# Kernel optimization log

Measured on AMD Instinct MI355X. Metric: run time of the kernel, lower is better.

Reference implementation:

```python
import jax, jax.numpy as jnp
import numpy as np

B, T, D, W = 2, 8192, 2048, 128  # batch, seq, n_embd, local_window
PAD = -1.0


def setup_inputs() -> dict:
    key = jax.random.key(0)
    k1, k2, k3 = jax.random.split(key, 3)
    x = jax.random.normal(k1, (B, T, D), jnp.float32)
    w_attn = jax.random.normal(k2, (3 * D, D), jnp.float32) * 0.02  # nn.Linear(n_embd, 3*n_embd)
    w_o = jax.random.normal(k3, (D, D), jnp.float32) * 0.02        # o_proj
    return {"x": x, "w_attn": w_attn, "w_o": w_o}


def reference(x, w_attn, w_o):
    Bn, Tn, Dn = x.shape
    w = Tn // W  # number of windows

    qkv = x @ w_attn.T                      # [B,T,3D]
    q, k, v = jnp.split(qkv, 3, axis=-1)
    q = q / W                               # q / config.local_window

    bq = q.reshape(Bn, w, W, Dn)
    bk = k.reshape(Bn, w, W, Dn)
    bv = v.reshape(Bn, w, W, Dn)

    # look_around(backward=1, forward=0, pad_value=-1): keys = [prev_window, cur_window]
    pad_blk = jnp.full((Bn, 1, W, Dn), PAD, dtype=x.dtype)
    bk_prev = jnp.concatenate([pad_blk, bk[:, :-1]], axis=1)
    bv_prev = jnp.concatenate([pad_blk, bv[:, :-1]], axis=1)
    bk2 = jnp.concatenate([bk_prev, bk], axis=2)  # [B,w,2W,D]
    bv2 = jnp.concatenate([bv_prev, bv], axis=2)  # [B,w,2W,D]

    # position indices
    t = jnp.arange(Tn, dtype=jnp.int32).reshape(w, W)
    t_prev = jnp.concatenate([jnp.full((1, W), -1, jnp.int32), t[:-1]], axis=0)
    tj = jnp.concatenate([t_prev, t], axis=1)     # [w,2W] key positions (-1 = pad)
    ti = t[:, :, None]                            # [w,W,1] query positions
    tjb = tj[:, None, :]                          # [w,1,2W]

    # masked where (ti < tj) | (ti > tj + W) | pad; masked sim -> 0 (not -inf; relu2, no softmax)
    keep = (ti >= tjb) & (ti <= tjb + W) & (tjb != -1)  # [w,W,2W]

    sim = jnp.einsum('bwie,bwje->bwij', bq, bk2)        # [B,w,W,2W]
    sim = jnp.where(keep[None], sim, 0.0)
    attn = jnp.square(jax.nn.relu(sim))                 # relu^2, no normalization
    out = jnp.einsum('bwij,bwje->bwie', attn, bv2)      # [B,w,W,D]
    out = out.reshape(Bn, Tn, Dn)
    return out @ w_o.T
```

## Files before the change

kernel.cpp:

```cpp
#include <hip/hip_runtime.h>
#include <stdint.h>
#include <stddef.h>

#define Bn 2
#define Tn 8192
#define Dn 2048

typedef unsigned short u16;
typedef unsigned int u32;
typedef __attribute__((ext_vector_type(8))) short short8;
typedef __attribute__((ext_vector_type(8))) unsigned short u16x8;
typedef __attribute__((ext_vector_type(4))) float f32x4;

__device__ __forceinline__ u16 f2bf(float f) {
  u32 x = __builtin_bit_cast(u32, f);
  x += 0x7fffu + ((x >> 16) & 1u);
  return (u16)(x >> 16);
}

__device__ __forceinline__ void gload16(void* lds, const void* g) {
  __builtin_amdgcn_global_load_lds(
      (const __attribute__((address_space(1))) u32*)g,
      (__attribute__((address_space(3))) u32*)lds, 16, 0, 0);
}

#define PH_BAR asm volatile("s_barrier" ::: "memory")
#define WAITV(N) asm volatile("s_waitcnt vmcnt(" #N ")" ::: "memory")

__global__ void cast_kernel(const float* __restrict__ in, u16* __restrict__ out, int n) {
  int stride = gridDim.x * blockDim.x;
  for (int i = blockIdx.x * blockDim.x + threadIdx.x; i < (n >> 2); i += stride) {
    float4 v = reinterpret_cast<const float4*>(in)[i];
    ushort4 o;
    o.x = f2bf(v.x); o.y = f2bf(v.y); o.z = f2bf(v.z); o.w = f2bf(v.w);
    reinterpret_cast<ushort4*>(out)[i] = o;
  }
}

template <int MODE>
__global__ __launch_bounds__(512, 2) void gemm256(
    const u16* __restrict__ Ag, const u16* __restrict__ Bg,
    u16* __restrict__ Oq, u16* __restrict__ Ok, u16* __restrict__ Ov,
    float* __restrict__ Of, int K) {
  __shared__ char sh[131072];
  const int tid = threadIdx.x, lane = tid & 63, wid = tid >> 6;
  const int wm = wid >> 2, wn = wid & 3;
  const int fr = lane & 15, kk = (lane >> 4) * 8;
  const int NT = K >> 6;

  int lin = blockIdx.y * 64 + blockIdx.x;
  int nwg = gridDim.x * gridDim.y;
  int lin2 = (lin & 7) * (nwg >> 3) + (lin >> 3);
  const int m0 = (lin2 & 63) * 256;
  const int n0 = (lin2 >> 6) * 256;

  const int rdoff = (fr * 128 + kk * 2) ^ (((fr >> 2) & 1) << 5);
  const int lq = (lane * 16) ^ (((lane >> 5) & 1) << 5);
  const int stgrow = wid * 8 + (lq >> 7);
  const int stgcol = (lq & 127) >> 1;

  auto stageA = [&](int db, int h, int tt) {
    const u16* s = Ag + (size_t)(m0 + h * 128 + stgrow) * K + tt * 64 + stgcol;
    char* d = sh + db * 32768 + h * 16384 + wid * 1024;
    gload16(d, s);
    gload16(d + 8192, s + (size_t)64 * K);
  };
  auto stageB = [&](int db, int h, int tt) {
    const u16* s = Bg + (size_t)(n0 + h * 128 + stgrow) * K + tt * 64 + stgcol;
    char* d = sh + 65536 + db * 32768 + h * 16384 + wid * 1024;
    gload16(d, s);
    gload16(d + 8192, s + (size_t)64 * K);
  };

  short8 a[4][2], b0[2][2], b1[2][2];
  f32x4 acc[8][4] = {};

  stageA(0, 0, 0); stageA(0, 1, 0); stageB(0, 0, 0); stageB(0, 1, 0);
  stageB(1, 0, 1); stageB(1, 1, 1);
  WAITV(4);
  PH_BAR;

  for (int t = 0; t < NT; ++t) {
    const int db = t & 1;
    const char* rdA = sh + db * 32768 + wm * 16384 + rdoff;
    const char* rdB = sh + 65536 + db * 32768 + (wn >> 1) * 16384 + (wn & 1) * 8192 + rdoff;

#pragma unroll
    for (int fm = 0; fm < 4; ++fm)
#pragma unroll
      for (int ks = 0; ks < 2; ++ks)
        a[fm][ks] = *(const short8*)(rdA + fm * 2048 + ks * 64);
#pragma unroll
    for (int fn = 0; fn < 2; ++fn)
#pragma unroll
      for (int ks = 0; ks < 2; ++ks)
        b0[fn][ks] = *(const short8*)(rdB + fn * 2048 + ks * 64);
    if (t + 1 < NT) stageA(db ^ 1, 0, t + 1);
    PH_BAR;
    __builtin_amdgcn_s_setprio(1);
#pragma unroll
    for (int fm = 0; fm < 4; ++fm)
#pragma unroll
      for (int fn = 0; fn < 2; ++fn)
#pragma unroll
        for (int ks = 0; ks < 2; ++ks)
          acc[fm][fn] = __builtin_amdgcn_mfma_f32_16x16x32_bf16(a[fm][ks], b0[fn][ks], acc[fm][fn], 0, 0, 0);
    __builtin_amdgcn_s_setprio(0);
    PH_BAR;

#pragma unroll
    for (int fn = 0; fn < 2; ++fn)
#pragma unroll
      for (int ks = 0; ks < 2; ++ks)
        b1[fn][ks] = *(const short8*)(rdB + (2 + fn) * 2048 + ks * 64);
    if (t + 1 < NT) stageA(db ^ 1, 1, t + 1);
    PH_BAR;
    __builtin_amdgcn_s_setprio(1);
#pragma unroll
    for (int fm = 0; fm < 4; ++fm)
#pragma unroll
      for (int fn = 0; fn < 2; ++fn)
#pragma unroll
        for (int ks = 0; ks < 2; ++ks)
          acc[fm][2 + fn] = __builtin_amdgcn_mfma_f32_16x16x32_bf16(a[fm][ks], b1[fn][ks], acc[fm][2 + fn], 0, 0, 0);
    __builtin_amdgcn_s_setprio(0);
    PH_BAR;

#pragma unroll
    for (int fm = 0; fm < 4; ++fm)
#pragma unroll
      for (int ks = 0; ks < 2; ++ks)
        a[fm][ks] = *(const short8*)(rdA + (4 + fm) * 2048 + ks * 64);
    if (t + 2 < NT) stageB(db, 0, t + 2);
    PH_BAR;
    __builtin_amdgcn_s_setprio(1);
#pragma unroll
    for (int fm = 0; fm < 4; ++fm)
#pragma unroll
      for (int fn = 0; fn < 2; ++fn)
#pragma unroll
        for (int ks = 0; ks < 2; ++ks)
          acc[4 + fm][fn] = __builtin_amdgcn_mfma_f32_16x16x32_bf16(a[fm][ks], b0[fn][ks], acc[4 + fm][fn], 0, 0, 0);
    __builtin_amdgcn_s_setprio(0);
    PH_BAR;

    if (t + 2 < NT) stageB(db, 1, t + 2);
    PH_BAR;
    __builtin_amdgcn_s_setprio(1);
#pragma unroll
    for (int fm = 0; fm < 4; ++fm)
#pragma unroll
      for (int fn = 0; fn < 2; ++fn)
#pragma unroll
        for (int ks = 0; ks < 2; ++ks)
          acc[4 + fm][2 + fn] = __builtin_amdgcn_mfma_f32_16x16x32_bf16(a[fm][ks], b1[fn][ks], acc[4 + fm][2 + fn], 0, 0, 0);
    __builtin_amdgcn_s_setprio(0);
    if (t + 2 < NT) { WAITV(4); }
    else if (t + 1 < NT) { WAITV(0); }
    PH_BAR;
  }

  const int ci = (lane >> 4) * 4;
  if (MODE == 0) {
    const int seg = n0 >> 11;
    u16* Cb = (seg == 0) ? Oq : ((seg == 1) ? Ok : Ov);
    const float scale = (seg == 0) ? (1.0f / 128.0f) : 1.0f;
    const int nl0 = n0 & (Dn - 1);
#pragma unroll
    for (int fm = 0; fm < 8; ++fm)
#pragma unroll
      for (int fn = 0; fn < 4; ++fn) {
        int row = m0 + wm * 128 + fm * 16 + ci;
        int col = nl0 + wn * 64 + fn * 16 + fr;
#pragma unroll
        for (int r = 0; r < 4; ++r)
          Cb[(size_t)(row + r) * Dn + col] = f2bf(acc[fm][fn][r] * scale);
      }
  } else {
#pragma unroll
    for (int fm = 0; fm < 8; ++fm)
#pragma unroll
      for (int fn = 0; fn < 4; ++fn) {
        int row = m0 + wm * 128 + fm * 16 + ci;
        int col = n0 + wn * 64 + fn * 16 + fr;
#pragma unroll
        for (int r = 0; r < 4; ++r)
          Of[(size_t)(row + r) * Dn + col] = acc[fm][fn][r];
      }
  }
}

__global__ __launch_bounds__(256) void transpose_kernel(
    const u16* __restrict__ vin, u16* __restrict__ vout) {
  __shared__ u16 tile[64][72];
  const int b = blockIdx.z;
  const int t0 = blockIdx.x * 64, d0 = blockIdx.y * 64;
  const int tid = threadIdx.x;
#pragma unroll
  for (int i = 0; i < 2; ++i) {
    int chunk = tid + i * 256;
    int row = chunk >> 3;
    int col = (chunk & 7) * 8;
    u16x8 v = *reinterpret_cast<const u16x8*>(
        vin + ((size_t)b * Tn + t0 + row) * Dn + d0 + col);
#pragma unroll
    for (int j = 0; j < 8; ++j) tile[row][col + j] = v[j];
  }
  __syncthreads();
#pragma unroll
  for (int i = 0; i < 2; ++i) {
    int chunk = tid + i * 256;
    int drow = chunk >> 3;
    int tcol = (chunk & 7) * 8;
    u16x8 v;
#pragma unroll
    for (int j = 0; j < 8; ++j) v[j] = tile[tcol + j][drow];
    *reinterpret_cast<u16x8*>(vout + ((size_t)b * Dn + d0 + drow) * Tn + t0 + tcol) = v;
  }
}

__global__ __launch_bounds__(512) void attn_kernel(
    const u16* __restrict__ q, const u16* __restrict__ k,
    const u16* __restrict__ vT, u16* __restrict__ ao) {
  __shared__ u16 sStage[16384];
  __shared__ u16 sP[128 * 264];
  u16* Qs = sStage;
  u16* Ks = sStage + 4096;
  u16* Vts = sStage;

  const int bid = blockIdx.x;
  const int b = bid >> 6, blk = bid & 63;
  const int tid = threadIdx.x, lane = tid & 63, wid = tid >> 6;
  const int tprev = blk * 128 - 128;

  const u16* qp = q + ((size_t)b * Tn + blk * 128) * Dn;
  const u16* kp = k + (size_t)b * Tn * Dn;
  const u16* vp = vT + (size_t)b * Dn * Tn;

  const int wm = wid >> 2, wn = wid & 3;
  const int srow = lane >> 2, scol = (lane & 3) * 8;
  const int fr = lane & 15, kk = (lane >> 4) * 8;

  f32x4 acc[4][4] = {};
  for (int k0 = 0; k0 < Dn; k0 += 32) {
    {
      int row = wid * 16 + srow;
      gload16(Qs + wid * 512, qp + (size_t)row * Dn + k0 + scol);
    }
#pragma unroll
    for (int i = 0; i < 2; ++i) {
      int chunk = wid * 2 + i;
      int j = chunk * 16 + srow;
      int trow = tprev + j;
      if (trow < 0) trow = 0;
      gload16(Ks + chunk * 512, kp + (size_t)trow * Dn + k0 + scol);
    }
    __syncthreads();
    short8 av[4], bv[4];
#pragma unroll
    for (int f = 0; f < 4; ++f) {
      av[f] = *reinterpret_cast<const short8*>(&Qs[(wm * 64 + f * 16 + fr) * 32 + kk]);
      bv[f] = *reinterpret_cast<const short8*>(&Ks[(wn * 64 + f * 16 + fr) * 32 + kk]);
    }
#pragma unroll
    for (int fm = 0; fm < 4; ++fm)
#pragma unroll
      for (int fn = 0; fn < 4; ++fn)
        acc[fm][fn] = __builtin_amdgcn_mfma_f32_16x16x32_bf16(av[fm], bv[fn], acc[fm][fn], 0, 0, 0);
    __syncthreads();
  }

  {
    const int ci = (lane >> 4) * 4;
#pragma unroll
    for (int fm = 0; fm < 4; ++fm)
#pragma unroll
      for (int fn = 0; fn < 4; ++fn)
#pragma unroll
        for (int r = 0; r < 4; ++r) {
          int i = wm * 64 + fm * 16 + ci + r;
          int j = wn * 64 + fn * 16 + fr;
          float s = acc[fm][fn][r];
          bool keep = (j < 128) ? (blk > 0 && i <= j) : (i >= j - 128);
          float p = (keep && s > 0.0f) ? s * s : 0.0f;
          sP[i * 264 + j] = f2bf(p);
        }
  }
  __syncthreads();

  for (int c = 0; c < 32; ++c) {
#pragma unroll
    for (int i = 0; i < 4; ++i) {
      int chunk = wid * 4 + i;
      int d = c * 64 + chunk * 2 + (lane >> 5);
      int t = tprev + (lane & 31) * 8;
      if (t < 0) t = 0;
      gload16(Vts + chunk * 512, vp + (size_t)d * Tn + t);
    }
    __syncthreads();
    f32x4 pacc[4] = {};
#pragma unroll
    for (int ks = 0; ks < 8; ++ks) {
      short8 a = *reinterpret_cast<const short8*>(&sP[(wid * 16 + fr) * 264 + ks * 32 + kk]);
#pragma unroll
      for (int fn = 0; fn < 4; ++fn) {
        short8 bv2 = *reinterpret_cast<const short8*>(&Vts[(fn * 16 + fr) * 256 + ks * 32 + kk]);
        pacc[fn] = __builtin_amdgcn_mfma_f32_16x16x32_bf16(a, bv2, pacc[fn], 0, 0, 0);
      }
    }
    const int ci = (lane >> 4) * 4;
    int trow = blk * 128 + wid * 16 + ci;
#pragma unroll
    for (int fn = 0; fn < 4; ++fn) {
      int d = c * 64 + fn * 16 + fr;
#pragma unroll
      for (int r = 0; r < 4; ++r)
        ao[((size_t)b * Tn + trow + r) * Dn + d] = f2bf(pacc[fn][r]);
    }
    __syncthreads();
  }
}

extern "C" void kernel_launch(void* const* d_in, const int* in_sizes, int n_in,
                              void* d_out, int out_size, void* d_ws, size_t ws_size,
                              hipStream_t stream) {
  const float* x = (const float*)d_in[0];
  const float* w_attn = (const float*)d_in[1];
  const float* w_o = (const float*)d_in[2];
  float* out = (float*)d_out;

  char* ws = (char*)d_ws;
  u16* xb  = (u16*)(ws + 0);
  u16* wb  = (u16*)(ws + 67108864);
  u16* wob = (u16*)(ws + 92274688);
  u16* qb  = (u16*)(ws + 100663296);
  u16* kb  = (u16*)(ws + 167772160);
  u16* vb  = (u16*)(ws + 234881024);
  u16* vTb = xb;
  u16* ao  = vb;

  cast_kernel<<<2048, 256, 0, stream>>>(x, xb, Bn * Tn * Dn);
  cast_kernel<<<1024, 256, 0, stream>>>(w_attn, wb, 3 * Dn * Dn);
  cast_kernel<<<512, 256, 0, stream>>>(w_o, wob, Dn * Dn);

  gemm256<0><<<dim3(64, 24), 512, 0, stream>>>(xb, wb, qb, kb, vb, nullptr, Dn);

  transpose_kernel<<<dim3(128, 32, 2), 256, 0, stream>>>(vb, vTb);

  attn_kernel<<<128, 512, 0, stream>>>(qb, kb, vTb, ao);

  gemm256<1><<<dim3(64, 8), 512, 0, stream>>>(ao, wob, nullptr, nullptr, nullptr, out, Dn);
}
```

Baseline: 1.030 ms.

## XOR-swizzle LDS layouts in GEMM and attention; widen attention QK k-step to 64

Replaces the LDS staging layouts in the GEMM and the attention kernel with an XOR swizzle of 16-byte chunks across rows, and adjusts the MFMA fragment read offsets to match. The aim is to cut LDS bank conflicts on the short8 fragment reads. The attention QK loop now steps 64 columns of K per iteration instead of 32, with a larger staging buffer, which halves the barrier count in that loop. The PV stage reads V tiles through the same swizzle. The new index math is intricate and a wrong swizzle would silently corrupt results.

```diff
diff --git a/kernel.cpp b/kernel.cpp
--- a/kernel.cpp
+++ b/kernel.cpp
@@ -45,7 +45,7 @@
   __shared__ char sh[131072];
   const int tid = threadIdx.x, lane = tid & 63, wid = tid >> 6;
   const int wm = wid >> 2, wn = wid & 3;
-  const int fr = lane & 15, kk = (lane >> 4) * 8;
+  const int fr = lane & 15;
   const int NT = K >> 6;
 
   int lin = blockIdx.y * 64 + blockIdx.x;
@@ -54,19 +54,23 @@
   const int m0 = (lin2 & 63) * 256;
   const int n0 = (lin2 >> 6) * 256;
 
-  const int rdoff = (fr * 128 + kk * 2) ^ (((fr >> 2) & 1) << 5);
-  const int lq = (lane * 16) ^ (((lane >> 5) & 1) << 5);
-  const int stgrow = wid * 8 + (lq >> 7);
-  const int stgcol = (lq & 127) >> 1;
+  const int frb2 = (fr >> 2) & 1;
+  const int kkb = (lane >> 4) * 16;
+  const int rdoff = fr * 128 + (kkb ^ ((fr & 3) << 4));
+  const int koff0 = frb2 * 64;
+  const int koff1 = 64 - koff0;
+
+  const int srow8 = lane >> 3;
+  const int scol8 = ((lane & 7) ^ srow8) * 8;
 
   auto stageA = [&](int db, int h, int tt) {
-    const u16* s = Ag + (size_t)(m0 + h * 128 + stgrow) * K + tt * 64 + stgcol;
+    const u16* s = Ag + (size_t)(m0 + h * 128 + wid * 8 + srow8) * K + tt * 64 + scol8;
     char* d = sh + db * 32768 + h * 16384 + wid * 1024;
     gload16(d, s);
     gload16(d + 8192, s + (size_t)64 * K);
   };
   auto stageB = [&](int db, int h, int tt) {
-    const u16* s = Bg + (size_t)(n0 + h * 128 + stgrow) * K + tt * 64 + stgcol;
+    const u16* s = Bg + (size_t)(n0 + h * 128 + wid * 8 + srow8) * K + tt * 64 + scol8;
     char* d = sh + 65536 + db * 32768 + h * 16384 + wid * 1024;
     gload16(d, s);
     gload16(d + 8192, s + (size_t)64 * K);
@@ -89,12 +93,12 @@
     for (int fm = 0; fm < 4; ++fm)
 #pragma unroll
       for (int ks = 0; ks < 2; ++ks)
-        a[fm][ks] = *(const short8*)(rdA + fm * 2048 + ks * 64);
+        a[fm][ks] = *(const short8*)(rdA + fm * 2048 + (ks ? koff1 : koff0));
 #pragma unroll
     for (int fn = 0; fn < 2; ++fn)
 #pragma unroll
       for (int ks = 0; ks < 2; ++ks)
-        b0[fn][ks] = *(const short8*)(rdB + fn * 2048 + ks * 64);
+        b0[fn][ks] = *(const short8*)(rdB + fn * 2048 + (ks ? koff1 : koff0));
     if (t + 1 < NT) stageA(db ^ 1, 0, t + 1);
     PH_BAR;
     __builtin_amdgcn_s_setprio(1);
@@ -112,7 +116,7 @@
     for (int fn = 0; fn < 2; ++fn)
 #pragma unroll
       for (int ks = 0; ks < 2; ++ks)
-        b1[fn][ks] = *(const short8*)(rdB + (2 + fn) * 2048 + ks * 64);
+        b1[fn][ks] = *(const short8*)(rdB + (2 + fn) * 2048 + (ks ? koff1 : koff0));
     if (t + 1 < NT) stageA(db ^ 1, 1, t + 1);
     PH_BAR;
     __builtin_amdgcn_s_setprio(1);
@@ -130,7 +134,7 @@
     for (int fm = 0; fm < 4; ++fm)
 #pragma unroll
       for (int ks = 0; ks < 2; ++ks)
-        a[fm][ks] = *(const short8*)(rdA + (4 + fm) * 2048 + ks * 64);
+        a[fm][ks] = *(const short8*)(rdA + (4 + fm) * 2048 + (ks ? koff1 : koff0));
     if (t + 2 < NT) stageB(db, 0, t + 2);
     PH_BAR;
     __builtin_amdgcn_s_setprio(1);
@@ -222,10 +226,10 @@
 __global__ __launch_bounds__(512) void attn_kernel(
     const u16* __restrict__ q, const u16* __restrict__ k,
     const u16* __restrict__ vT, u16* __restrict__ ao) {
-  __shared__ u16 sStage[16384];
+  __shared__ u16 sStage[24576];
   __shared__ u16 sP[128 * 264];
   u16* Qs = sStage;
-  u16* Ks = sStage + 4096;
+  u16* Ks = sStage + 8192;
   u16* Vts = sStage;
 
   const int bid = blockIdx.x;
@@ -238,35 +242,49 @@
   const u16* vp = vT + (size_t)b * Dn * Tn;
 
   const int wm = wid >> 2, wn = wid & 3;
-  const int srow = lane >> 2, scol = (lane & 3) * 8;
-  const int fr = lane & 15, kk = (lane >> 4) * 8;
+  const int fr = lane & 15;
+  const int kkb = (lane >> 4) * 16;
+
+  const int frb2 = (fr >> 2) & 1;
+  const int rdoff = fr * 128 + (kkb ^ ((fr & 3) << 4));
+  const int koff0 = frb2 * 64;
+  const int koff1 = 64 - koff0;
+  const int srow8 = lane >> 3;
+  const int scol8 = ((lane & 7) ^ srow8) * 8;
 
   f32x4 acc[4][4] = {};
-  for (int k0 = 0; k0 < Dn; k0 += 32) {
-    {
-      int row = wid * 16 + srow;
-      gload16(Qs + wid * 512, qp + (size_t)row * Dn + k0 + scol);
-    }
+  for (int k0 = 0; k0 < Dn; k0 += 64) {
 #pragma unroll
     for (int i = 0; i < 2; ++i) {
       int chunk = wid * 2 + i;
-      int j = chunk * 16 + srow;
-      int trow = tprev + j;
+      int row = chunk * 8 + srow8;
+      gload16((char*)Qs + chunk * 1024, qp + (size_t)row * Dn + k0 + scol8);
+    }
+#pragma unroll
+    for (int i = 0; i < 4; ++i) {
+      int chunk = wid * 4 + i;
+      int trow = tprev + chunk * 8 + srow8;
       if (trow < 0) trow = 0;
-      gload16(Ks + chunk * 512, kp + (size_t)trow * Dn + k0 + scol);
+      gload16((char*)Ks + chunk * 1024, kp + (size_t)trow * Dn + k0 + scol8);
     }
     __syncthreads();
-    short8 av[4], bv[4];
-#pragma unroll
-    for (int f = 0; f < 4; ++f) {
-      av[f] = *reinterpret_cast<const short8*>(&Qs[(wm * 64 + f * 16 + fr) * 32 + kk]);
-      bv[f] = *reinterpret_cast<const short8*>(&Ks[(wn * 64 + f * 16 + fr) * 32 + kk]);
-    }
+    short8 av[4][2], bv[4][2];
+    const char* qbase = (const char*)Qs + wm * 8192 + rdoff;
+    const char* kbase = (const char*)Ks + wn * 8192 + rdoff;
+#pragma unroll
+    for (int f = 0; f < 4; ++f)
+#pragma unroll
+      for (int ks = 0; ks < 2; ++ks) {
+        av[f][ks] = *(const short8*)(qbase + f * 2048 + (ks ? koff1 : koff0));
+        bv[f][ks] = *(const short8*)(kbase + f * 2048 + (ks ? koff1 : koff0));
+      }
 #pragma unroll
     for (int fm = 0; fm < 4; ++fm)
 #pragma unroll
       for (int fn = 0; fn < 4; ++fn)
-        acc[fm][fn] = __builtin_amdgcn_mfma_f32_16x16x32_bf16(av[fm], bv[fn], acc[fm][fn], 0, 0, 0);
+#pragma unroll
+        for (int ks = 0; ks < 2; ++ks)
+          acc[fm][fn] = __builtin_amdgcn_mfma_f32_16x16x32_bf16(av[fm][ks], bv[fn][ks], acc[fm][fn], 0, 0, 0);
     __syncthreads();
   }
 
@@ -288,23 +306,29 @@
   }
   __syncthreads();
 
+  const int vrow_c = lane >> 5;
   for (int c = 0; c < 32; ++c) {
 #pragma unroll
     for (int i = 0; i < 4; ++i) {
       int chunk = wid * 4 + i;
-      int d = c * 64 + chunk * 2 + (lane >> 5);
-      int t = tprev + (lane & 31) * 8;
+      int row = chunk * 2 + vrow_c;
+      int d = c * 64 + row;
+      int t = tprev + (((lane & 31) ^ (row & 7)) * 8);
       if (t < 0) t = 0;
-      gload16(Vts + chunk * 512, vp + (size_t)d * Tn + t);
+      gload16((char*)Vts + chunk * 1024, vp + (size_t)d * Tn + t);
     }
     __syncthreads();
     f32x4 pacc[4] = {};
+    const char* vb0 = (const char*)Vts + fr * 512 + (kkb ^ ((fr & 3) << 4)) + koff0;
+    const char* vb1 = (const char*)Vts + fr * 512 + (kkb ^ ((fr & 3) << 4)) + koff1;
+    const char* pbase = (const char*)sP + (wid * 16 + fr) * 528 + kkb;
 #pragma unroll
     for (int ks = 0; ks < 8; ++ks) {
-      short8 a = *reinterpret_cast<const short8*>(&sP[(wid * 16 + fr) * 264 + ks * 32 + kk]);
+      short8 a = *(const short8*)(pbase + ks * 64);
 #pragma unroll
       for (int fn = 0; fn < 4; ++fn) {
-        short8 bv2 = *reinterpret_cast<const short8*>(&Vts[(fn * 16 + fr) * 256 + ks * 32 + kk]);
+        const char* vb = ((ks & 1) ? vb1 : vb0) + fn * 8192 + (ks >> 1) * 128;
+        short8 bv2 = *(const short8*)vb;
         pacc[fn] = __builtin_amdgcn_mfma_f32_16x16x32_bf16(a, bv2, pacc[fn], 0, 0, 0);
       }
     }
```

After: 911.1 us. -11.6%, faster.
